# Performance work log

Measured on AMD Instinct MI355X. Metric: run time of the kernel, lower is better.

## Reference

```python
import jax, jax.numpy as jnp
import numpy as np

V_PER_MESH = 6596
HIDDEN = 128
# per-body-part clamp limits from the original module (parts 1..14)
LIMITS = jnp.array([0.04, 0.06, 0.04, 0.04, 0.02, 0.02, 0.04, 0.04,
                    0.03, 0.03, 0.02, 0.02, 0.01, 0.01], dtype=jnp.float32)


def setup_inputs() -> dict:
    key = jax.random.key(0)
    ks = jax.random.split(key, 16)
    B, V, H = 32, V_PER_MESH, HIDDEN
    N = B * V
    E = 3 * N
    inp = {}
    inp["verts"] = jax.random.normal(ks[0], (N, 3), jnp.float32)
    inp["normals"] = jax.random.normal(ks[1], (N, 3), jnp.float32)
    inp["anchor_v"] = jax.random.uniform(ks[2], (V, 3), jnp.float32)
    inp["edges"] = jax.random.randint(ks[3], (E, 2), 0, N)
    inp["part_id"] = jax.random.randint(ks[4], (V,), 0, 14)
    dims = [3, H + 3, H + 3]  # first gconv sees only vert normals (vert_feat_dim=0)
    i = 5
    for l, d in enumerate(dims):
        s = 1.0 / np.sqrt(d)
        inp[f"w0_{l}"] = jax.random.normal(ks[i], (d, H), jnp.float32) * s; i += 1
        inp[f"b0_{l}"] = jnp.zeros((H,), jnp.float32)
        inp[f"w1_{l}"] = jax.random.normal(ks[i], (d, H), jnp.float32) * s; i += 1
        inp[f"b1_{l}"] = jnp.zeros((H,), jnp.float32)
    inp["w_off"] = jax.random.normal(ks[i], (H + 3, 3), jnp.float32) * 0.01
    inp["b_off"] = jnp.zeros((3,), jnp.float32)
    return inp


def _forward(verts, normals, anchor_v, edges, part_id, layers, w_off, b_off):
    N = verts.shape[0]
    B = N // V_PER_MESH
    e0, e1 = edges[:, 0], edges[:, 1]
    feats = normals  # vert_pos_packed (verts_normals_packed), vert_feats=None
    for (w0, b0, w1, b1) in layers:
        x0 = feats @ w0 + b0            # [N,H] self transform
        x1 = feats @ w1 + b1            # [N,H] neighbor transform
        # undirected gather-scatter over mesh edges
        nbr = jnp.zeros_like(x0).at[e0].add(x1[e1]).at[e1].add(x1[e0])
        h = jax.nn.relu(x0 + nbr)       # vert_feats_nopos
        feats = jnp.concatenate([h, normals], axis=1)  # [N,H+3]
    deform = jnp.tanh(feats @ w_off + b_off)  # [N,3]
    # per-body-part clamp, vectorized: one limit per vertex, tiled over meshes
    lim = jnp.tile(LIMITS[part_id], B)[:, None]          # [N,1]
    clamped = jnp.clip(deform, -lim, lim)
    anchor = jnp.tile(anchor_v, (B, 1))                  # [N,3]
    new_verts = verts + clamped * anchor                 # offset_verts
    return new_verts, h


def reference(verts, normals, anchor_v, edges, part_id,
              w0_0, b0_0, w1_0, b1_0,
              w0_1, b0_1, w1_1, b1_1,
              w0_2, b0_2, w1_2, b1_2,
              w_off, b_off):
    layers = [(w0_0, b0_0, w1_0, b1_0),
              (w0_1, b0_1, w1_1, b1_1),
              (w0_2, b0_2, w1_2, b1_2)]
    return _forward(verts, normals, anchor_v, edges, part_id, layers, w_off, b_off)
```

## Files before the change

kernel.cpp:

```cpp
#include <hip/hip_runtime.h>

#define N_TOT 211072
#define V_MESH 6596
#define E_TOT 633216
#define CAP 32
#define KP 184
#define KSTEPS 5
#define MM3_BPM 207
#define FUS_BPM 413
#define FIN_BPM 1649

typedef __attribute__((ext_vector_type(8))) short bf16x8;
typedef __attribute__((ext_vector_type(4))) float f32x4;

__constant__ float c_LIM[14] = {0.04f,0.06f,0.04f,0.04f,0.02f,0.02f,0.04f,0.04f,
                                0.03f,0.03f,0.02f,0.02f,0.01f,0.01f};

__device__ __forceinline__ unsigned f2bf(float f) {
    unsigned x = __float_as_uint(f);
    return (x + 0x7fffu + ((x >> 16) & 1u)) >> 16;
}
__device__ __forceinline__ float bflo(unsigned u) { return __uint_as_float(u << 16); }
__device__ __forceinline__ float bfhi(unsigned u) { return __uint_as_float(u & 0xffff0000u); }
__device__ __forceinline__ unsigned pk_trunc(float a0, float a1) {
    return __builtin_amdgcn_perm(__float_as_uint(a1), __float_as_uint(a0), 0x07060302u);
}

__global__ __launch_bounds__(256) void fill_adj_kernel(const int* __restrict__ edges,
                                                       int* __restrict__ cnt,
                                                       int* __restrict__ adj) {
    int e = blockIdx.x * 256 + threadIdx.x;
    if (e >= E_TOT) return;
    int2 ed = ((const int2*)edges)[e];
    int p0 = atomicAdd(&cnt[ed.x], 1);
    if (p0 < CAP) adj[(size_t)ed.x * CAP + p0] = ed.y;
    int p1 = atomicAdd(&cnt[ed.y], 1);
    if (p1 < CAP) adj[(size_t)ed.y * CAP + p1] = ed.x;
}

__global__ __launch_bounds__(256) void pad_adj_kernel(const int* __restrict__ cnt,
                                                      int* __restrict__ adj) {
    int i = blockIdx.x * 256 + threadIdx.x;
    if (i >= N_TOT) return;
    int deg = cnt[i]; if (deg > CAP) deg = CAP;
    int end = (deg <= 8) ? 8 : ((deg + 7) & ~7);
    if (end > CAP) end = CAP;
    for (int k = deg; k < end; ++k) adj[(size_t)i * CAP + k] = N_TOT;
}

__global__ __launch_bounds__(256) void conv_w_kernel(const float* __restrict__ w0,
                                                     const float* __restrict__ b0,
                                                     const float* __restrict__ w1,
                                                     const float* __restrict__ b1,
                                                     short* __restrict__ Wt,
                                                     float* __restrict__ bb) {
    int c = blockIdx.x;
    int k = threadIdx.x;
    const float* w = (c < 128) ? w0 : w1;
    int cc = c & 127;
    if (k < KP) {
        unsigned val = (k < 131) ? f2bf(w[(size_t)k * 128 + cc]) : 0u;
        Wt[(size_t)c * KP + k] = (short)val;
    }
    if (k == 0) bb[c] = (c < 128) ? b0[cc] : b1[cc];
}

__global__ __launch_bounds__(256) void mm3_kernel(const float* __restrict__ normals,
                                                  const float* __restrict__ w0,
                                                  const float* __restrict__ b0,
                                                  const float* __restrict__ w1,
                                                  const float* __restrict__ b1,
                                                  unsigned* __restrict__ xc) {
    __shared__ float nL[32][3];
    int t = threadIdx.x;
    int d = blockIdx.x, tt = d >> 3;
    int m  = (d & 7) + 8 * (tt / MM3_BPM);
    int r0 = (tt % MM3_BPM) * 32;
    int base = m * V_MESH;
    if (t < 96) {
        int r = t / 3, k = t - r * 3;
        int rr = r0 + r; if (rr >= V_MESH) rr = V_MESH - 1;
        nL[r][k] = normals[(size_t)(base + rr) * 3 + k];
    }
    __syncthreads();
    int mm = (t >> 6) & 1;
    int rh = t >> 7;
    int c2 = t & 63;
    const float* w = mm ? w1 : w0;
    const float* b = mm ? b1 : b0;
    float wA0 = w[0*128 + 2*c2],     wA1 = w[1*128 + 2*c2],     wA2 = w[2*128 + 2*c2];
    float wB0 = w[0*128 + 2*c2 + 1], wB1 = w[1*128 + 2*c2 + 1], wB2 = w[2*128 + 2*c2 + 1];
    float bA = b[2*c2], bB = b[2*c2 + 1];
    #pragma unroll
    for (int r = 0; r < 16; ++r) {
        int lr = rh * 16 + r;
        if (r0 + lr < V_MESH) {
            float vA = bA + nL[lr][0]*wA0 + nL[lr][1]*wA1 + nL[lr][2]*wA2;
            float vB = bB + nL[lr][0]*wB0 + nL[lr][1]*wB1 + nL[lr][2]*wB2;
            xc[(size_t)(base + r0 + lr) * 128 + mm * 64 + c2] = f2bf(vA) | (f2bf(vB) << 16);
        }
    }
}

__global__ __launch_bounds__(1024, 8) void fused_kernel(const unsigned* __restrict__ xc_in,
                                                        const float* __restrict__ normals,
                                                        const int* __restrict__ cnt,
                                                        const int* __restrict__ adj,
                                                        const short* __restrict__ Wt,
                                                        const float* __restrict__ bb,
                                                        unsigned* __restrict__ xc_out) {
    __shared__ short tileA[16 * KP];
    __shared__ short tileC[16 * 256];
    int tid  = threadIdx.x;
    int w    = tid >> 6;
    int lane = tid & 63;
    int g    = lane >> 4;
    int ln   = lane & 15;

    int d  = blockIdx.x, tt = d >> 3;
    int m  = (d & 7) + 8 * (tt / FUS_BPM);
    int r16 = (tt % FUS_BPM) * 16;
    int base = m * V_MESH;
    bool valid = (r16 + w) < V_MESH;
    int i = base + (valid ? r16 + w : V_MESH - 1);

    int deg0 = cnt[i];
    int jv = (lane < CAP) ? adj[(size_t)i * CAP + lane] : (int)N_TOT;
    unsigned selfu = xc_in[(size_t)i * 128 + lane];
    float nv = (lane < 3) ? normals[(size_t)i * 3 + lane] : 0.f;
    int cb = w * 16;
    float bv = bb[cb + ln];
    bf16x8 bfrag[KSTEPS];
    #pragma unroll
    for (int kk = 0; kk < KSTEPS; ++kk)
        bfrag[kk] = *(const bf16x8*)(Wt + (size_t)(cb + ln) * KP + kk * 32 + g * 8);

    const unsigned* x1b = xc_in + 64 + lane;
    unsigned u[8];
    #pragma unroll
    for (int q = 0; q < 8; ++q) {
        int j = __builtin_amdgcn_readlane(jv, q);
        u[q] = x1b[(size_t)j * 128];
    }
    float a0 = bflo(selfu), a1 = bfhi(selfu);
    float d0 = 0.f, d1 = 0.f;
    #pragma unroll
    for (int q = 0; q < 8; q += 2) {
        a0 += bflo(u[q]);     a1 += bfhi(u[q]);
        d0 += bflo(u[q + 1]); d1 += bfhi(u[q + 1]);
    }
    int deg = (deg0 > CAP) ? CAP : deg0;
    deg = __builtin_amdgcn_readfirstlane(deg);
    for (int bq = 8; bq < deg; bq += 8) {
        unsigned v[8];
        #pragma unroll
        for (int q = 0; q < 8; ++q) {
            int j = __builtin_amdgcn_readlane(jv, bq + q);
            v[q] = x1b[(size_t)j * 128];
        }
        #pragma unroll
        for (int q = 0; q < 8; q += 2) {
            a0 += bflo(v[q]);     a1 += bfhi(v[q]);
            d0 += bflo(v[q + 1]); d1 += bfhi(v[q + 1]);
        }
    }
    a0 = fmaxf(a0 + d0, 0.f);
    a1 = fmaxf(a1 + d1, 0.f);

    ((unsigned*)tileA)[w * (KP / 2) + lane] = pk_trunc(a0, a1);
    unsigned nb = f2bf(nv);
    unsigned nb0 = __shfl((int)nb, 0), nb1 = __shfl((int)nb, 1), nb2 = __shfl((int)nb, 2);
    if (lane < 16) {
        unsigned v = (lane == 0) ? (nb0 | (nb1 << 16)) : (lane == 1) ? nb2 : 0u;
        ((unsigned*)tileA)[w * (KP / 2) + 64 + lane] = v;
    }
    __syncthreads();

    f32x4 acc = {bv, bv, bv, bv};
    #pragma unroll
    for (int kk = 0; kk < KSTEPS; ++kk) {
        bf16x8 af = *(const bf16x8*)(tileA + ln * KP + kk * 32 + g * 8);
        acc = __builtin_amdgcn_mfma_f32_16x16x32_bf16(af, bfrag[kk], acc, 0, 0, 0);
    }
    #pragma unroll
    for (int j = 0; j < 4; ++j) {
        float po = __shfl_xor(acc[j], 1);
        if (!(ln & 1)) {
            unsigned pk = f2bf(acc[j]) | (f2bf(po) << 16);
            int dd = w * 8 + (ln >> 1);
            int row = g * 4 + j;
            ((unsigned*)tileC)[row * 128 + (dd ^ (g << 3))] = pk;
        }
    }
    __syncthreads();

    if (valid) {
        int key = (w >> 2) << 3;
        ushort4 v4 = *(const ushort4*)&((unsigned*)tileC)[w * 128 + ((2 * lane) ^ key)];
        ((ushort4*)(xc_out + (size_t)i * 128))[lane] = v4;
    }
}

__global__ __launch_bounds__(256) void final_fused_kernel(const unsigned* __restrict__ xc_in,
                                                          const int* __restrict__ cnt,
                                                          const int* __restrict__ adj,
                                                          const float* __restrict__ normals,
                                                          const float* __restrict__ verts,
                                                          const float* __restrict__ anchor_v,
                                                          const int* __restrict__ part_id,
                                                          const float* __restrict__ w_off,
                                                          const float* __restrict__ b_off,
                                                          float* __restrict__ hout,
                                                          float* __restrict__ out_verts) {
    __shared__ float wo[131 * 3];
    for (int t = threadIdx.x; t < 131 * 3; t += 256) wo[t] = w_off[t];
    __syncthreads();
    int tid  = threadIdx.x;
    int w    = tid >> 6;
    int lane = tid & 63;
    int d  = blockIdx.x, tt = d >> 3;
    int m  = (d & 7) + 8 * (tt / FIN_BPM);
    int i  = m * V_MESH + (tt % FIN_BPM) * 4 + w;

    int deg0 = cnt[i];
    int jv = (lane < CAP) ? adj[(size_t)i * CAP + lane] : (int)N_TOT;
    unsigned selfu = xc_in[(size_t)i * 128 + lane];

    const unsigned* x1b = xc_in + 64 + lane;
    unsigned u[8];
    #pragma unroll
    for (int q = 0; q < 8; ++q) {
        int j = __builtin_amdgcn_readlane(jv, q);
        u[q] = x1b[(size_t)j * 128];
    }
    float a0 = bflo(selfu), a1 = bfhi(selfu);
    float d0 = 0.f, d1 = 0.f;
    #pragma unroll
    for (int q = 0; q < 8; q += 2) {
        a0 += bflo(u[q]);     a1 += bfhi(u[q]);
        d0 += bflo(u[q + 1]); d1 += bfhi(u[q + 1]);
    }
    int deg = (deg0 > CAP) ? CAP : deg0;
    deg = __builtin_amdgcn_readfirstlane(deg);
    for (int bq = 8; bq < deg; bq += 8) {
        unsigned v[8];
        #pragma unroll
        for (int q = 0; q < 8; ++q) {
            int j = __builtin_amdgcn_readlane(jv, bq + q);
            v[q] = x1b[(size_t)j * 128];
        }
        #pragma unroll
        for (int q = 0; q < 8; q += 2) {
            a0 += bflo(v[q]);     a1 += bfhi(v[q]);
            d0 += bflo(v[q + 1]); d1 += bfhi(v[q + 1]);
        }
    }
    a0 = fmaxf(a0 + d0, 0.f);
    a1 = fmaxf(a1 + d1, 0.f);

    float2 hv; hv.x = a0; hv.y = a1;
    ((float2*)(hout + (size_t)i * 128))[lane] = hv;

    int cA = 2 * lane, cB = 2 * lane + 1;
    float s0 = a0 * wo[cA * 3 + 0] + a1 * wo[cB * 3 + 0];
    float s1 = a0 * wo[cA * 3 + 1] + a1 * wo[cB * 3 + 1];
    float s2 = a0 * wo[cA * 3 + 2] + a1 * wo[cB * 3 + 2];
    #pragma unroll
    for (int dd = 32; dd; dd >>= 1) {
        s0 += __shfl_xor(s0, dd);
        s1 += __shfl_xor(s1, dd);
        s2 += __shfl_xor(s2, dd);
    }
    if (lane < 3) {
        int v = i % V_MESH;
        float n0 = normals[(size_t)i * 3 + 0];
        float n1 = normals[(size_t)i * 3 + 1];
        float n2 = normals[(size_t)i * 3 + 2];
        float s = (lane == 0) ? s0 : (lane == 1) ? s1 : s2;
        s += n0 * wo[128 * 3 + lane] + n1 * wo[129 * 3 + lane] + n2 * wo[130 * 3 + lane];
        s += b_off[lane];
        float dd2 = tanhf(s);
        float lim = c_LIM[part_id[v]];
        dd2 = fminf(fmaxf(dd2, -lim), lim);
        out_verts[(size_t)i * 3 + lane] =
            verts[(size_t)i * 3 + lane] + dd2 * anchor_v[(size_t)v * 3 + lane];
    }
}

extern "C" void kernel_launch(void* const* d_in, const int* in_sizes, int n_in,
                              void* d_out, int out_size, void* d_ws, size_t ws_size,
                              hipStream_t stream) {
    const float* verts    = (const float*)d_in[0];
    const float* normals  = (const float*)d_in[1];
    const float* anchor_v = (const float*)d_in[2];
    const int*   edges    = (const int*)d_in[3];
    const int*   part_id  = (const int*)d_in[4];
    const float* w0_0 = (const float*)d_in[5];
    const float* b0_0 = (const float*)d_in[6];
    const float* w1_0 = (const float*)d_in[7];
    const float* b1_0 = (const float*)d_in[8];
    const float* w0_1 = (const float*)d_in[9];
    const float* b0_1 = (const float*)d_in[10];
    const float* w1_1 = (const float*)d_in[11];
    const float* b1_1 = (const float*)d_in[12];
    const float* w0_2 = (const float*)d_in[13];
    const float* b0_2 = (const float*)d_in[14];
    const float* w1_2 = (const float*)d_in[15];
    const float* b1_2 = (const float*)d_in[16];
    const float* w_off = (const float*)d_in[17];
    const float* b_off = (const float*)d_in[18];

    float* out_verts = (float*)d_out;
    float* hout = (float*)d_out + (size_t)3 * N_TOT;

    unsigned* xcB = (unsigned*)d_out;

    char* p = (char*)d_ws;
    unsigned* xcA = (unsigned*)p;  p += (size_t)(N_TOT + 1) * 128 * 4;
    int*   cnt = (int*)p;          p += (size_t)N_TOT * 4;
    int*   adj = (int*)p;          p += (size_t)N_TOT * CAP * 4;
    short* Wt1 = (short*)p;        p += 256 * KP * 2;
    float* bb1 = (float*)p;        p += 256 * 4;
    short* Wt2 = (short*)p;        p += 256 * KP * 2;
    float* bb2 = (float*)p;

    hipMemsetAsync(cnt, 0, (size_t)N_TOT * 4, stream);
    hipMemsetAsync(xcA + (size_t)N_TOT * 128, 0, 512, stream);
    hipMemsetAsync(xcB + (size_t)N_TOT * 128, 0, 512, stream);
    fill_adj_kernel<<<(E_TOT + 255) / 256, 256, 0, stream>>>(edges, cnt, adj);
    pad_adj_kernel<<<(N_TOT + 255) / 256, 256, 0, stream>>>(cnt, adj);
    conv_w_kernel<<<256, 256, 0, stream>>>(w0_1, b0_1, w1_1, b1_1, Wt1, bb1);
    conv_w_kernel<<<256, 256, 0, stream>>>(w0_2, b0_2, w1_2, b1_2, Wt2, bb2);

    mm3_kernel<<<8 * 4 * MM3_BPM, 256, 0, stream>>>(normals, w0_0, b0_0, w1_0, b1_0, xcA);
    fused_kernel<<<8 * 4 * FUS_BPM, 1024, 0, stream>>>(xcA, normals, cnt, adj, Wt1, bb1, xcB);
    fused_kernel<<<8 * 4 * FUS_BPM, 1024, 0, stream>>>(xcB, normals, cnt, adj, Wt2, bb2, xcA);
    final_fused_kernel<<<8 * 4 * FIN_BPM, 256, 0, stream>>>(xcA, cnt, adj, normals, verts,
                                                            anchor_v, part_id, w_off, b_off,
                                                            hout, out_verts);
}
```

Measured before the change: 468.3 us.

## Fuse first graph-conv layer by aggregating neighbor normals before the 3-wide transform

The first layer's neighbor sum is computed on the 3-component normals, using linearity (sum of x@W1+b1 equals (sum x)@W1 + deg*b1). This removes the mm3 kernel and one full 128-wide bf16 gather pass over the feature buffer, fusing layer 1 with the layer-2 matmul. It also adds a padded float4 normals buffer, pads all adjacency slots to CAP so each lane gathers directly, and uses hardware packed bf16 conversion. Other changes: grid indexing becomes linear instead of mesh-interleaved, and the next neighbor gathers are hoisted earlier. Rounding differs slightly from the reference order (sum then transform, rounding instead of truncation).

```diff
diff --git a/kernel.cpp b/kernel.cpp
--- a/kernel.cpp
+++ b/kernel.cpp
@@ -6,9 +6,6 @@
 #define CAP 32
 #define KP 184
 #define KSTEPS 5
-#define MM3_BPM 207
-#define FUS_BPM 413
-#define FIN_BPM 1649
 
 typedef __attribute__((ext_vector_type(8))) short bf16x8;
 typedef __attribute__((ext_vector_type(4))) float f32x4;
@@ -22,8 +19,10 @@
 }
 __device__ __forceinline__ float bflo(unsigned u) { return __uint_as_float(u << 16); }
 __device__ __forceinline__ float bfhi(unsigned u) { return __uint_as_float(u & 0xffff0000u); }
-__device__ __forceinline__ unsigned pk_trunc(float a0, float a1) {
-    return __builtin_amdgcn_perm(__float_as_uint(a1), __float_as_uint(a0), 0x07060302u);
+__device__ __forceinline__ unsigned cvt_pk_bf16(float lo, float hi) {
+    unsigned r;
+    asm("v_cvt_pk_bf16_f32 %0, %1, %2" : "=v"(r) : "v"(lo), "v"(hi));
+    return r;
 }
 
 __global__ __launch_bounds__(256) void fill_adj_kernel(const int* __restrict__ edges,
@@ -43,9 +42,20 @@
     int i = blockIdx.x * 256 + threadIdx.x;
     if (i >= N_TOT) return;
     int deg = cnt[i]; if (deg > CAP) deg = CAP;
-    int end = (deg <= 8) ? 8 : ((deg + 7) & ~7);
-    if (end > CAP) end = CAP;
-    for (int k = deg; k < end; ++k) adj[(size_t)i * CAP + k] = N_TOT;
+    for (int k = deg; k < CAP; ++k) adj[(size_t)i * CAP + k] = N_TOT;
+}
+
+__global__ __launch_bounds__(256) void prep_nrm4_kernel(const float* __restrict__ normals,
+                                                        float4* __restrict__ nrm4) {
+    int i = blockIdx.x * 256 + threadIdx.x;
+    if (i > N_TOT) return;
+    float4 v = {0.f, 0.f, 0.f, 0.f};
+    if (i < N_TOT) {
+        v.x = normals[(size_t)i * 3 + 0];
+        v.y = normals[(size_t)i * 3 + 1];
+        v.z = normals[(size_t)i * 3 + 2];
+    }
+    nrm4[i] = v;
 }
 
 __global__ __launch_bounds__(256) void conv_w_kernel(const float* __restrict__ w0,
@@ -65,45 +75,102 @@
     if (k == 0) bb[c] = (c < 128) ? b0[cc] : b1[cc];
 }
 
-__global__ __launch_bounds__(256) void mm3_kernel(const float* __restrict__ normals,
-                                                  const float* __restrict__ w0,
-                                                  const float* __restrict__ b0,
-                                                  const float* __restrict__ w1,
-                                                  const float* __restrict__ b1,
-                                                  unsigned* __restrict__ xc) {
-    __shared__ float nL[32][3];
-    int t = threadIdx.x;
-    int d = blockIdx.x, tt = d >> 3;
-    int m  = (d & 7) + 8 * (tt / MM3_BPM);
-    int r0 = (tt % MM3_BPM) * 32;
-    int base = m * V_MESH;
-    if (t < 96) {
-        int r = t / 3, k = t - r * 3;
-        int rr = r0 + r; if (rr >= V_MESH) rr = V_MESH - 1;
-        nL[r][k] = normals[(size_t)(base + rr) * 3 + k];
-    }
-    __syncthreads();
-    int mm = (t >> 6) & 1;
-    int rh = t >> 7;
-    int c2 = t & 63;
-    const float* w = mm ? w1 : w0;
-    const float* b = mm ? b1 : b0;
-    float wA0 = w[0*128 + 2*c2],     wA1 = w[1*128 + 2*c2],     wA2 = w[2*128 + 2*c2];
-    float wB0 = w[0*128 + 2*c2 + 1], wB1 = w[1*128 + 2*c2 + 1], wB2 = w[2*128 + 2*c2 + 1];
-    float bA = b[2*c2], bB = b[2*c2 + 1];
-    #pragma unroll
-    for (int r = 0; r < 16; ++r) {
-        int lr = rh * 16 + r;
-        if (r0 + lr < V_MESH) {
-            float vA = bA + nL[lr][0]*wA0 + nL[lr][1]*wA1 + nL[lr][2]*wA2;
-            float vB = bB + nL[lr][0]*wB0 + nL[lr][1]*wB1 + nL[lr][2]*wB2;
-            xc[(size_t)(base + r0 + lr) * 128 + mm * 64 + c2] = f2bf(vA) | (f2bf(vB) << 16);
-        }
-    }
+__global__ __launch_bounds__(1024, 8) void fused1_kernel(const float4* __restrict__ nrm4,
+                                                         const int* __restrict__ cnt,
+                                                         const int* __restrict__ adj,
+                                                         const float* __restrict__ w0,
+                                                         const float* __restrict__ b0,
+                                                         const float* __restrict__ w1,
+                                                         const float* __restrict__ b1,
+                                                         const short* __restrict__ Wt,
+                                                         const float* __restrict__ bb,
+                                                         unsigned* __restrict__ xc_out) {
+    __shared__ short tileA[16 * KP];
+    __shared__ short tileC[16 * 256];
+    __shared__ float wL[2][3][128];
+    __shared__ float bL[2][128];
+
+    int tid  = threadIdx.x;
+    int w    = tid >> 6;
+    int lane = tid & 63;
+    int g    = lane >> 4;
+    int ln   = lane & 15;
+    int row0 = blockIdx.x * 16;
+    int i    = row0 + w;
+
+    if (tid < 768) {
+        int mm = tid / 384, r = tid - mm * 384;
+        (&wL[mm][0][0])[r] = (mm ? w1 : w0)[r];
+    } else {
+        int t2 = tid - 768;
+        if (t2 < 256) bL[t2 >> 7][t2 & 127] = ((t2 >> 7) ? b1 : b0)[t2 & 127];
+    }
+
+    int deg0 = cnt[i];
+    int jv = (lane < CAP) ? adj[(size_t)i * CAP + lane] : (int)N_TOT;
+    float4 self4 = nrm4[i];
+    float4 nj = nrm4[jv];
+
+    int deg = (deg0 > CAP) ? CAP : deg0;
+    deg = __builtin_amdgcn_readfirstlane(deg);
+    float degf = (float)deg;
+
+    float sx = nj.x, sy = nj.y, sz = nj.z;
+    #pragma unroll
+    for (int d = 1; d < 64; d <<= 1) {
+        sx += __shfl_xor(sx, d);
+        sy += __shfl_xor(sy, d);
+        sz += __shfl_xor(sz, d);
+    }
+    __syncthreads();
+
+    int c0 = 2 * lane, c1 = 2 * lane + 1;
+    float h0 = bL[0][c0] + degf * bL[1][c0]
+             + self4.x * wL[0][0][c0] + self4.y * wL[0][1][c0] + self4.z * wL[0][2][c0]
+             + sx * wL[1][0][c0] + sy * wL[1][1][c0] + sz * wL[1][2][c0];
+    float h1 = bL[0][c1] + degf * bL[1][c1]
+             + self4.x * wL[0][0][c1] + self4.y * wL[0][1][c1] + self4.z * wL[0][2][c1]
+             + sx * wL[1][0][c1] + sy * wL[1][1][c1] + sz * wL[1][2][c1];
+    h0 = fmaxf(h0, 0.f);
+    h1 = fmaxf(h1, 0.f);
+
+    unsigned* tA32 = (unsigned*)tileA;
+    tA32[w * (KP / 2) + lane] = cvt_pk_bf16(h0, h1);
+    if (lane < 16) {
+        unsigned v = (lane == 0) ? cvt_pk_bf16(self4.x, self4.y)
+                   : (lane == 1) ? cvt_pk_bf16(self4.z, 0.f) : 0u;
+        tA32[w * (KP / 2) + 64 + lane] = v;
+    }
+    __syncthreads();
+
+    int cb = w * 16;
+    float bv = bb[cb + ln];
+    f32x4 acc = {bv, bv, bv, bv};
+    #pragma unroll
+    for (int kk = 0; kk < KSTEPS; ++kk) {
+        bf16x8 bf = *(const bf16x8*)(Wt + (size_t)(cb + ln) * KP + kk * 32 + g * 8);
+        bf16x8 af = *(const bf16x8*)(tileA + ln * KP + kk * 32 + g * 8);
+        acc = __builtin_amdgcn_mfma_f32_16x16x32_bf16(af, bf, acc, 0, 0, 0);
+    }
+    #pragma unroll
+    for (int j = 0; j < 4; ++j) {
+        float po = __shfl_xor(acc[j], 1);
+        if (!(ln & 1)) {
+            unsigned pk = cvt_pk_bf16(acc[j], po);
+            int dd = w * 8 + (ln >> 1);
+            int row = g * 4 + j;
+            ((unsigned*)tileC)[row * 128 + (dd ^ (g << 3))] = pk;
+        }
+    }
+    __syncthreads();
+
+    int key = (w >> 2) << 3;
+    ushort4 v4 = *(const ushort4*)&((unsigned*)tileC)[w * 128 + ((2 * lane) ^ key)];
+    ((ushort4*)(xc_out + (size_t)(row0 + w) * 128))[lane] = v4;
 }
 
 __global__ __launch_bounds__(1024, 8) void fused_kernel(const unsigned* __restrict__ xc_in,
-                                                        const float* __restrict__ normals,
+                                                        const float4* __restrict__ nrm4,
                                                         const int* __restrict__ cnt,
                                                         const int* __restrict__ adj,
                                                         const short* __restrict__ Wt,
@@ -116,18 +183,21 @@
     int lane = tid & 63;
     int g    = lane >> 4;
     int ln   = lane & 15;
-
-    int d  = blockIdx.x, tt = d >> 3;
-    int m  = (d & 7) + 8 * (tt / FUS_BPM);
-    int r16 = (tt % FUS_BPM) * 16;
-    int base = m * V_MESH;
-    bool valid = (r16 + w) < V_MESH;
-    int i = base + (valid ? r16 + w : V_MESH - 1);
+    int row0 = blockIdx.x * 16;
+    int i    = row0 + w;
 
     int deg0 = cnt[i];
     int jv = (lane < CAP) ? adj[(size_t)i * CAP + lane] : (int)N_TOT;
+
+    const unsigned* x1b = xc_in + 64 + lane;
+    unsigned u[8];
+    #pragma unroll
+    for (int q = 0; q < 8; ++q) {
+        int j = __builtin_amdgcn_readlane(jv, q);
+        u[q] = x1b[(size_t)j * 128];
+    }
     unsigned selfu = xc_in[(size_t)i * 128 + lane];
-    float nv = (lane < 3) ? normals[(size_t)i * 3 + lane] : 0.f;
+    float4 self4 = nrm4[i];
     int cb = w * 16;
     float bv = bb[cb + ln];
     bf16x8 bfrag[KSTEPS];
@@ -135,13 +205,6 @@
     for (int kk = 0; kk < KSTEPS; ++kk)
         bfrag[kk] = *(const bf16x8*)(Wt + (size_t)(cb + ln) * KP + kk * 32 + g * 8);
 
-    const unsigned* x1b = xc_in + 64 + lane;
-    unsigned u[8];
-    #pragma unroll
-    for (int q = 0; q < 8; ++q) {
-        int j = __builtin_amdgcn_readlane(jv, q);
-        u[q] = x1b[(size_t)j * 128];
-    }
     float a0 = bflo(selfu), a1 = bfhi(selfu);
     float d0 = 0.f, d1 = 0.f;
     #pragma unroll
@@ -167,12 +230,12 @@
     a0 = fmaxf(a0 + d0, 0.f);
     a1 = fmaxf(a1 + d1, 0.f);
 
-    ((unsigned*)tileA)[w * (KP / 2) + lane] = pk_trunc(a0, a1);
-    unsigned nb = f2bf(nv);
-    unsigned nb0 = __shfl((int)nb, 0), nb1 = __shfl((int)nb, 1), nb2 = __shfl((int)nb, 2);
+    unsigned* tA32 = (unsigned*)tileA;
+    tA32[w * (KP / 2) + lane] = cvt_pk_bf16(a0, a1);
     if (lane < 16) {
-        unsigned v = (lane == 0) ? (nb0 | (nb1 << 16)) : (lane == 1) ? nb2 : 0u;
-        ((unsigned*)tileA)[w * (KP / 2) + 64 + lane] = v;
+        unsigned v = (lane == 0) ? cvt_pk_bf16(self4.x, self4.y)
+                   : (lane == 1) ? cvt_pk_bf16(self4.z, 0.f) : 0u;
+        tA32[w * (KP / 2) + 64 + lane] = v;
     }
     __syncthreads();
 
@@ -186,7 +249,7 @@
     for (int j = 0; j < 4; ++j) {
         float po = __shfl_xor(acc[j], 1);
         if (!(ln & 1)) {
-            unsigned pk = f2bf(acc[j]) | (f2bf(po) << 16);
+            unsigned pk = cvt_pk_bf16(acc[j], po);
             int dd = w * 8 + (ln >> 1);
             int row = g * 4 + j;
             ((unsigned*)tileC)[row * 128 + (dd ^ (g << 3))] = pk;
@@ -194,11 +257,9 @@
     }
     __syncthreads();
 
-    if (valid) {
-        int key = (w >> 2) << 3;
-        ushort4 v4 = *(const ushort4*)&((unsigned*)tileC)[w * 128 + ((2 * lane) ^ key)];
-        ((ushort4*)(xc_out + (size_t)i * 128))[lane] = v4;
-    }
+    int key = (w >> 2) << 3;
+    ushort4 v4 = *(const ushort4*)&((unsigned*)tileC)[w * 128 + ((2 * lane) ^ key)];
+    ((ushort4*)(xc_out + (size_t)(row0 + w) * 128))[lane] = v4;
 }
 
 __global__ __launch_bounds__(256) void final_fused_kernel(const unsigned* __restrict__ xc_in,
@@ -218,9 +279,7 @@
     int tid  = threadIdx.x;
     int w    = tid >> 6;
     int lane = tid & 63;
-    int d  = blockIdx.x, tt = d >> 3;
-    int m  = (d & 7) + 8 * (tt / FIN_BPM);
-    int i  = m * V_MESH + (tt % FIN_BPM) * 4 + w;
+    int i    = blockIdx.x * 4 + w;
 
     int deg0 = cnt[i];
     int jv = (lane < CAP) ? adj[(size_t)i * CAP + lane] : (int)N_TOT;
@@ -317,25 +376,27 @@
 
     char* p = (char*)d_ws;
     unsigned* xcA = (unsigned*)p;  p += (size_t)(N_TOT + 1) * 128 * 4;
-    int*   cnt = (int*)p;          p += (size_t)N_TOT * 4;
-    int*   adj = (int*)p;          p += (size_t)N_TOT * CAP * 4;
-    short* Wt1 = (short*)p;        p += 256 * KP * 2;
-    float* bb1 = (float*)p;        p += 256 * 4;
-    short* Wt2 = (short*)p;        p += 256 * KP * 2;
-    float* bb2 = (float*)p;
+    int*   cnt  = (int*)p;         p += (size_t)N_TOT * 4;
+    int*   adj  = (int*)p;         p += (size_t)N_TOT * CAP * 4;
+    short* Wt1  = (short*)p;       p += 256 * KP * 2;
+    float* bb1  = (float*)p;       p += 256 * 4;
+    short* Wt2  = (short*)p;       p += 256 * KP * 2;
+    float* bb2  = (float*)p;       p += 256 * 4;
+    float4* nrm4 = (float4*)p;     p += (size_t)(N_TOT + 1) * 16;
 
     hipMemsetAsync(cnt, 0, (size_t)N_TOT * 4, stream);
     hipMemsetAsync(xcA + (size_t)N_TOT * 128, 0, 512, stream);
     hipMemsetAsync(xcB + (size_t)N_TOT * 128, 0, 512, stream);
     fill_adj_kernel<<<(E_TOT + 255) / 256, 256, 0, stream>>>(edges, cnt, adj);
     pad_adj_kernel<<<(N_TOT + 255) / 256, 256, 0, stream>>>(cnt, adj);
+    prep_nrm4_kernel<<<(N_TOT + 256) / 256, 256, 0, stream>>>(normals, nrm4);
     conv_w_kernel<<<256, 256, 0, stream>>>(w0_1, b0_1, w1_1, b1_1, Wt1, bb1);
     conv_w_kernel<<<256, 256, 0, stream>>>(w0_2, b0_2, w1_2, b1_2, Wt2, bb2);
 
-    mm3_kernel<<<8 * 4 * MM3_BPM, 256, 0, stream>>>(normals, w0_0, b0_0, w1_0, b1_0, xcA);
-    fused_kernel<<<8 * 4 * FUS_BPM, 1024, 0, stream>>>(xcA, normals, cnt, adj, Wt1, bb1, xcB);
-    fused_kernel<<<8 * 4 * FUS_BPM, 1024, 0, stream>>>(xcB, normals, cnt, adj, Wt2, bb2, xcA);
-    final_fused_kernel<<<8 * 4 * FIN_BPM, 256, 0, stream>>>(xcA, cnt, adj, normals, verts,
-                                                            anchor_v, part_id, w_off, b_off,
-                                                            hout, out_verts);
-}
+    fused1_kernel<<<N_TOT / 16, 1024, 0, stream>>>(nrm4, cnt, adj, w0_0, b0_0, w1_0, b1_0,
+                                                   Wt1, bb1, xcB);
+    fused_kernel<<<N_TOT / 16, 1024, 0, stream>>>(xcB, nrm4, cnt, adj, Wt2, bb2, xcA);
+    final_fused_kernel<<<N_TOT / 4, 256, 0, stream>>>(xcA, cnt, adj, normals, verts,
+                                                      anchor_v, part_id, w_off, b_off,
+                                                      hout, out_verts);
+}
```

After: 501.5 us. +7.1%, slower.
